# Kernel tuning notes

Hardware: AMD Instinct MI355X
Metric: run time of the kernel (lower is better)

## Reference

```python
import jax, jax.numpy as jnp
import numpy as np

D_MODEL = 1024
NUM_HEADS = 16
HEAD_DIM = D_MODEL // NUM_HEADS


def setup_inputs() -> dict:
    key = jax.random.key(0)
    k_x, k_wqkv, k_bqkv, k_wo, k_bo = jax.random.split(key, 5)
    s = 1.0 / np.sqrt(D_MODEL)
    return {
        "x": jax.random.normal(k_x, (4, 2048, D_MODEL), dtype=jnp.float32),
        "W_qkv": jax.random.uniform(k_wqkv, (D_MODEL, 3 * D_MODEL), jnp.float32, -s, s),
        "b_qkv": jax.random.uniform(k_bqkv, (3 * D_MODEL,), jnp.float32, -s, s),
        "W_out": jax.random.uniform(k_wo, (D_MODEL, D_MODEL), jnp.float32, -s, s),
        "b_out": jax.random.uniform(k_bo, (D_MODEL,), jnp.float32, -s, s),
    }


def reference(x, W_qkv, b_qkv, W_out, b_out):
    B, N, C = x.shape
    # fused QKV projection -> [B, N, 3, H, Dh]
    qkv = (x @ W_qkv + b_qkv).reshape(B, N, 3, NUM_HEADS, HEAD_DIM)
    q = jnp.transpose(qkv[:, :, 0], (0, 2, 1, 3))  # [B, H, N, Dh]
    k = jnp.transpose(qkv[:, :, 1], (0, 2, 1, 3))
    v = jnp.transpose(qkv[:, :, 2], (0, 2, 1, 3))
    scale = 1.0 / jnp.sqrt(jnp.asarray(HEAD_DIM, dtype=x.dtype))
    attn = jnp.einsum('bhqd,bhkd->bhqk', q, k) * scale  # [B, H, N, N]
    attn = jax.nn.softmax(attn, axis=-1)
    # dropout is identity in eval mode
    out = jnp.einsum('bhqk,bhkd->bhqd', attn, v)  # [B, H, N, Dh]
    out = jnp.transpose(out, (0, 2, 1, 3)).reshape(B, N, C)
    return out @ W_out + b_out
```

## Files before the change

### kernel.cpp

```cpp
#include <hip/hip_runtime.h>


typedef __bf16 bf16x8 __attribute__((ext_vector_type(8)));
typedef float f32x4 __attribute__((ext_vector_type(4)));

#define DEV __device__ __forceinline__

DEV unsigned short f2b(float x) {
  unsigned int u = __float_as_uint(x);
  u += 0x7fffu + ((u >> 16) & 1u);
  return (unsigned short)(u >> 16);
}

DEV unsigned int pk_bf16(float a, float b) {
  unsigned int ua = __float_as_uint(a) + 0x8000u;
  unsigned int ub = __float_as_uint(b) + 0x8000u;
  return __builtin_amdgcn_perm(ub, ua, 0x07060302u);
}

#if __has_builtin(__builtin_amdgcn_exp2f)
DEV float exp2_fast(float x) { return __builtin_amdgcn_exp2f(x); }
#else
DEV float exp2_fast(float x) { return exp2f(x); }
#endif

DEV void g2l16(const void* g, void* l) {
  __builtin_amdgcn_global_load_lds(
      (const __attribute__((address_space(1))) unsigned int*)(unsigned long long)g,
      (__attribute__((address_space(3))) unsigned int*)(unsigned int)(unsigned long long)l,
      16, 0, 0);
}

__global__ void cvt_x_kernel(const float* __restrict__ x,
                             unsigned short* __restrict__ xb) {
  int i = blockIdx.x * blockDim.x + threadIdx.x;
  float4 v = ((const float4*)x)[i];
  ushort4 o;
  o.x = f2b(v.x); o.y = f2b(v.y); o.z = f2b(v.z); o.w = f2b(v.w);
  ((ushort4*)xb)[i] = o;
}

__global__ void cvt_wt_kernel(const float* __restrict__ W,
                              unsigned short* __restrict__ Wt,
                              int K, int N) {
  __shared__ float tile[32][33];
  int n0 = blockIdx.x * 32, k0 = blockIdx.y * 32;
  int tx = threadIdx.x, ty = threadIdx.y;
#pragma unroll
  for (int i = 0; i < 32; i += 8)
    tile[ty + i][tx] = W[(size_t)(k0 + ty + i) * N + n0 + tx];
  __syncthreads();
#pragma unroll
  for (int i = 0; i < 32; i += 8)
    Wt[(size_t)(n0 + ty + i) * K + k0 + tx] = f2b(tile[tx][ty + i]);
}

#define QSCALE 0.18033688011112042f

template <int MODE>
__global__ __launch_bounds__(256, 2)
void gemm_bt_kernel(const unsigned short* __restrict__ A,
                    const unsigned short* __restrict__ Bt,
                    const float* __restrict__ bias,
                    unsigned short* __restrict__ qout,
                    unsigned short* __restrict__ kfrout,
                    unsigned short* __restrict__ vfrout,
                    float* __restrict__ fout) {
  constexpr int K = 1024;
  __shared__ unsigned short As[128 * 32];
  __shared__ unsigned short Bs[128 * 32];

  const int tid = threadIdx.x;
  const int lane = tid & 63;
  const int w = tid >> 6;
  const int wm = w & 1, wn = w >> 1;
  const int l15 = lane & 15, quad = lane >> 4;
  const int m0 = blockIdx.y * 128;
  const int n0 = blockIdx.x * 128;

  const unsigned short* Ag = A + (size_t)m0 * K;
  const unsigned short* Bg = Bt + (size_t)n0 * K;

  const int c0 = tid, c1 = tid + 256;
  const size_t ga0 = (size_t)(c0 >> 2) * K + (size_t)(c0 & 3) * 8;
  const size_t ga1 = (size_t)(c1 >> 2) * K + (size_t)(c1 & 3) * 8;
  unsigned short* la0 = &As[c0 * 8];
  unsigned short* la1 = &As[c1 * 8];
  unsigned short* lb0 = &Bs[c0 * 8];
  unsigned short* lb1 = &Bs[c1 * 8];

  f32x4 acc[4][4] = {};

  for (int kt = 0; kt < K; kt += 32) {
    g2l16(Ag + ga0 + kt, la0);
    g2l16(Ag + ga1 + kt, la1);
    g2l16(Bg + ga0 + kt, lb0);
    g2l16(Bg + ga1 + kt, lb1);
    __syncthreads();
    bf16x8 af[4], bfr[4];
#pragma unroll
    for (int i = 0; i < 4; ++i) {
      af[i]  = *(const bf16x8*)&As[(wm * 64 + i * 16 + l15) * 32 + quad * 8];
      bfr[i] = *(const bf16x8*)&Bs[(wn * 64 + i * 16 + l15) * 32 + quad * 8];
    }
#pragma unroll
    for (int mi = 0; mi < 4; ++mi)
#pragma unroll
      for (int ni = 0; ni < 4; ++ni)
        acc[mi][ni] = __builtin_amdgcn_mfma_f32_16x16x32_bf16(
            af[mi], bfr[ni], acc[mi][ni], 0, 0, 0);
    __syncthreads();
  }

  float bv[4];
#pragma unroll
  for (int ni = 0; ni < 4; ++ni)
    bv[ni] = bias[n0 + wn * 64 + ni * 16 + l15];

  if (MODE == 0) {
    const int sel = n0 >> 10;
    const int bbat = m0 >> 11;
    const int ktb = ((m0 & 2047) >> 6) + wm;
    if (sel == 0) {
#pragma unroll
      for (int mi = 0; mi < 4; ++mi) {
        int rb = m0 + wm * 64 + mi * 16 + quad * 4;
#pragma unroll
        for (int ni = 0; ni < 4; ++ni) {
          int c = (n0 & 1023) + wn * 64 + ni * 16 + l15;
#pragma unroll
          for (int r = 0; r < 4; ++r)
            qout[(size_t)(rb + r) * 1024 + c] =
                f2b((acc[mi][ni][r] + bv[ni]) * QSCALE);
        }
      }
    } else if (sel == 1) {
#pragma unroll
      for (int ni = 0; ni < 4; ++ni) {
        int c = (n0 & 1023) + wn * 64 + ni * 16 + l15;
        int h = c >> 6, d = c & 63;
        int kc = d >> 5, dq = (d >> 3) & 3, j = d & 7;
        size_t fb = ((((size_t)(bbat * 16 + h) * 32 + ktb) * 8) + kc) * 512 +
                    (size_t)(dq * 16) * 8 + j;
#pragma unroll
        for (int mi = 0; mi < 4; ++mi) {
          size_t fm = fb + (size_t)mi * 1024;
#pragma unroll
          for (int r = 0; r < 4; ++r)
            kfrout[fm + (quad * 4 + r) * 8] = f2b(acc[mi][ni][r] + bv[ni]);
        }
      }
    } else {
      const int fqb = quad >> 1;
      const int jj0 = (quad & 1) * 4;
#pragma unroll
      for (int ni = 0; ni < 4; ++ni) {
        int c = (n0 & 1023) + wn * 64 + ni * 16 + l15;
        int h = c >> 6, d = c & 63;
        int df = d >> 4, fl15 = d & 15;
#pragma unroll
        for (int mi = 0; mi < 4; ++mi) {
          int kc2 = mi >> 1;
          int fquad = (mi & 1) * 2 + fqb;
          size_t fb = ((((size_t)(bbat * 16 + h) * 32 + ktb) * 8) + df * 2 + kc2) * 512 +
                      (size_t)(fquad * 16 + fl15) * 8 + jj0;
          ushort4 pk;
          pk.x = f2b(acc[mi][ni][0] + bv[ni]);
          pk.y = f2b(acc[mi][ni][1] + bv[ni]);
          pk.z = f2b(acc[mi][ni][2] + bv[ni]);
          pk.w = f2b(acc[mi][ni][3] + bv[ni]);
          *(ushort4*)&vfrout[fb] = pk;
        }
      }
    }
  } else {
#pragma unroll
    for (int mi = 0; mi < 4; ++mi) {
      int rb = m0 + wm * 64 + mi * 16 + quad * 4;
#pragma unroll
      for (int ni = 0; ni < 4; ++ni) {
        int c = n0 + wn * 64 + ni * 16 + l15;
#pragma unroll
        for (int r = 0; r < 4; ++r)
          fout[(size_t)(rb + r) * 1024 + c] = acc[mi][ni][r] + bv[ni];
      }
    }
  }
}

__global__ __launch_bounds__(256, 2)
void attn_kernel(const unsigned short* __restrict__ qg,
                 const unsigned short* __restrict__ kfr,
                 const unsigned short* __restrict__ vfr,
                 unsigned short* __restrict__ oat) {
  __shared__ unsigned short pt[256 * 72];

  const int tid = threadIdx.x;
  const int lane = tid & 63;
  const int w = tid >> 6;
  const int l15 = lane & 15, quad = lane >> 4;

  const int head = blockIdx.x * 8 + (blockIdx.y >> 3);
  const int q0 = (blockIdx.y & 7) * 256;
  const int b = head >> 4, h = head & 15;
  const size_t tokbase = (size_t)b * 2048;

  bf16x8 qf[4][2];
#pragma unroll
  for (int ni = 0; ni < 4; ++ni)
#pragma unroll
    for (int kc = 0; kc < 2; ++kc) {
      int q = q0 + w * 64 + ni * 16 + l15;
      qf[ni][kc] = *(const bf16x8*)(qg + (tokbase + q) * 1024 + h * 64 +
                                    kc * 32 + quad * 8);
    }

  f32x4 oacc[4][4] = {};
  float lsum[4] = {0.f, 0.f, 0.f, 0.f};

  const bf16x8* kp = (const bf16x8*)kfr + (size_t)head * 32 * 512;
  const bf16x8* vp = (const bf16x8*)vfr + (size_t)head * 32 * 512;
  const int qrow = w * 64 + l15;

  bf16x8 kfA[8], vfA[8];
#pragma unroll
  for (int f = 0; f < 8; ++f) {
    kfA[f] = kp[f * 64 + lane];
    vfA[f] = vp[f * 64 + lane];
  }

  for (int kt = 0; kt < 32; ++kt) {
    bf16x8 kfB[8], vfB[8];
    if (kt < 31) {
      const bf16x8* kn = kp + (kt + 1) * 512;
      const bf16x8* vn = vp + (kt + 1) * 512;
#pragma unroll
      for (int f = 0; f < 8; ++f) {
        kfB[f] = kn[f * 64 + lane];
        vfB[f] = vn[f * 64 + lane];
      }
    }

#pragma unroll
    for (int nh = 0; nh < 2; ++nh) {
      f32x4 st[4][2];
#pragma unroll
      for (int mi = 0; mi < 4; ++mi)
#pragma unroll
        for (int nj = 0; nj < 2; ++nj) {
          f32x4 a = {0.f, 0.f, 0.f, 0.f};
          a = __builtin_amdgcn_mfma_f32_16x16x32_bf16(kfA[mi * 2 + 0], qf[nh * 2 + nj][0], a, 0, 0, 0);
          a = __builtin_amdgcn_mfma_f32_16x16x32_bf16(kfA[mi * 2 + 1], qf[nh * 2 + nj][1], a, 0, 0, 0);
          st[mi][nj] = a;
        }
#pragma unroll
      for (int nj = 0; nj < 2; ++nj) {
        int ni = nh * 2 + nj;
        float rs = 0.f;
#pragma unroll
        for (int mi = 0; mi < 4; ++mi) {
          float p0 = exp2_fast(st[mi][nj][0]);
          float p1 = exp2_fast(st[mi][nj][1]);
          float p2 = exp2_fast(st[mi][nj][2]);
          float p3 = exp2_fast(st[mi][nj][3]);
          rs += (p0 + p1) + (p2 + p3);
          uint2 pw;
          pw.x = pk_bf16(p0, p1);
          pw.y = pk_bf16(p2, p3);
          *(uint2*)&pt[(qrow + ni * 16) * 72 + mi * 16 + quad * 4] = pw;
        }
        lsum[ni] += rs;
      }
    }

    bf16x8 pf[4][2];
#pragma unroll
    for (int ni = 0; ni < 4; ++ni)
#pragma unroll
      for (int kc = 0; kc < 2; ++kc)
        pf[ni][kc] = *(const bf16x8*)&pt[(qrow + ni * 16) * 72 + kc * 32 + quad * 8];
#pragma unroll
    for (int df = 0; df < 4; ++df)
#pragma unroll
      for (int kc = 0; kc < 2; ++kc)
#pragma unroll
        for (int ni = 0; ni < 4; ++ni)
          oacc[df][ni] = __builtin_amdgcn_mfma_f32_16x16x32_bf16(
              vfA[df * 2 + kc], pf[ni][kc], oacc[df][ni], 0, 0, 0);

#pragma unroll
    for (int f = 0; f < 8; ++f) { kfA[f] = kfB[f]; vfA[f] = vfB[f]; }
  }

#pragma unroll
  for (int ni = 0; ni < 4; ++ni) {
    float s = lsum[ni];
    s += __shfl_xor(s, 16, 64);
    s += __shfl_xor(s, 32, 64);
    float inv = __builtin_amdgcn_rcpf(s);
    int q = q0 + w * 64 + ni * 16 + l15;
#pragma unroll
    for (int df = 0; df < 4; ++df) {
      uint2 pw;
      pw.x = pk_bf16(oacc[df][ni][0] * inv, oacc[df][ni][1] * inv);
      pw.y = pk_bf16(oacc[df][ni][2] * inv, oacc[df][ni][3] * inv);
      *(uint2*)&oat[(tokbase + q) * 1024 + h * 64 + df * 16 + quad * 4] = pw;
    }
  }
}

extern "C" void kernel_launch(void* const* d_in, const int* in_sizes, int n_in,
                              void* d_out, int out_size, void* d_ws, size_t ws_size,
                              hipStream_t stream) {
  const float* x    = (const float*)d_in[0];
  const float* Wqkv = (const float*)d_in[1];
  const float* bqkv = (const float*)d_in[2];
  const float* Wout = (const float*)d_in[3];
  const float* bout = (const float*)d_in[4];
  float* out = (float*)d_out;

  char* ws = (char*)d_ws;
  unsigned short* xb  = (unsigned short*)(ws + (size_t)0);
  unsigned short* wqt = (unsigned short*)(ws + ((size_t)16 << 20));
  unsigned short* wot = (unsigned short*)(ws + ((size_t)22 << 20));
  unsigned short* qbf = (unsigned short*)(ws + ((size_t)24 << 20));
  unsigned short* kfr = (unsigned short*)(ws + ((size_t)40 << 20));
  unsigned short* vfr = (unsigned short*)(ws + ((size_t)56 << 20));
  unsigned short* oat = (unsigned short*)(ws + ((size_t)72 << 20));

  cvt_x_kernel<<<8192, 256, 0, stream>>>(x, xb);
  cvt_wt_kernel<<<dim3(96, 32), dim3(32, 8), 0, stream>>>(Wqkv, wqt, 1024, 3072);
  cvt_wt_kernel<<<dim3(32, 32), dim3(32, 8), 0, stream>>>(Wout, wot, 1024, 1024);

  gemm_bt_kernel<0><<<dim3(24, 64), 256, 0, stream>>>(
      xb, wqt, bqkv, qbf, kfr, vfr, nullptr);

  attn_kernel<<<dim3(8, 64), 256, 0, stream>>>(qbf, kfr, vfr, oat);

  gemm_bt_kernel<1><<<dim3(8, 64), 256, 0, stream>>>(
      oat, wot, bout, nullptr, nullptr, nullptr, out);
}
```

Measured before the change: 277.6 us.

## Transpose softmax probabilities in registers with permlane swaps instead of LDS

```diff
diff --git a/kernel.cpp b/kernel.cpp
--- a/kernel.cpp
+++ b/kernel.cpp
@@ -3,6 +3,7 @@
 
 typedef __bf16 bf16x8 __attribute__((ext_vector_type(8)));
 typedef float f32x4 __attribute__((ext_vector_type(4)));
+typedef unsigned int u32x4 __attribute__((ext_vector_type(4)));
 
 #define DEV __device__ __forceinline__
 
@@ -23,6 +24,34 @@
 #else
 DEV float exp2_fast(float x) { return exp2f(x); }
 #endif
+
+DEV void xpose_pair(unsigned int a, unsigned int b,
+                    unsigned int& x, unsigned int& y) {
+#if __has_builtin(__builtin_amdgcn_permlane32_swap) && \
+    __has_builtin(__builtin_amdgcn_permlane16_swap)
+  auto t = __builtin_amdgcn_permlane32_swap(a, b, false, false);
+  auto u = __builtin_amdgcn_permlane16_swap(t[0], t[1], false, false);
+  x = u[0];
+  y = u[1];
+#else
+  int la = (int)(threadIdx.x & 63);
+  unsigned int a32 = (unsigned int)__shfl_xor((int)a, 32, 64);
+  unsigned int b32 = (unsigned int)__shfl_xor((int)b, 32, 64);
+  unsigned int t0 = (la < 32) ? a : b32;
+  unsigned int t1 = (la < 32) ? a32 : b;
+  unsigned int t0x = (unsigned int)__shfl_xor((int)t0, 16, 64);
+  unsigned int t1x = (unsigned int)__shfl_xor((int)t1, 16, 64);
+  bool odd = ((la >> 4) & 1) != 0;
+  x = odd ? t1x : t0;
+  y = odd ? t1 : t0x;
+#endif
+}
+
+DEV bf16x8 u4_to_bf(u32x4 v) {
+  union { u32x4 u; bf16x8 b; } c;
+  c.u = v;
+  return c.b;
+}
 
 DEV void g2l16(const void* g, void* l) {
   __builtin_amdgcn_global_load_lds(
@@ -193,8 +222,6 @@
                  const unsigned short* __restrict__ kfr,
                  const unsigned short* __restrict__ vfr,
                  unsigned short* __restrict__ oat) {
-  __shared__ unsigned short pt[256 * 72];
-
   const int tid = threadIdx.x;
   const int lane = tid & 63;
   const int w = tid >> 6;
@@ -220,7 +247,6 @@
 
   const bf16x8* kp = (const bf16x8*)kfr + (size_t)head * 32 * 512;
   const bf16x8* vp = (const bf16x8*)vfr + (size_t)head * 32 * 512;
-  const int qrow = w * 64 + l15;
 
   bf16x8 kfA[8], vfA[8];
 #pragma unroll
@@ -229,6 +255,7 @@
     vfA[f] = vp[f * 64 + lane];
   }
 
+#pragma unroll 2
   for (int kt = 0; kt < 32; ++kt) {
     bf16x8 kfB[8], vfB[8];
     if (kt < 31) {
@@ -247,16 +274,23 @@
 #pragma unroll
       for (int mi = 0; mi < 4; ++mi)
 #pragma unroll
-        for (int nj = 0; nj < 2; ++nj) {
-          f32x4 a = {0.f, 0.f, 0.f, 0.f};
-          a = __builtin_amdgcn_mfma_f32_16x16x32_bf16(kfA[mi * 2 + 0], qf[nh * 2 + nj][0], a, 0, 0, 0);
-          a = __builtin_amdgcn_mfma_f32_16x16x32_bf16(kfA[mi * 2 + 1], qf[nh * 2 + nj][1], a, 0, 0, 0);
-          st[mi][nj] = a;
-        }
+        for (int nj = 0; nj < 2; ++nj)
+          st[mi][nj] = (f32x4){0.f, 0.f, 0.f, 0.f};
+#pragma unroll
+      for (int kc = 0; kc < 2; ++kc)
+#pragma unroll
+        for (int mi = 0; mi < 4; ++mi)
+#pragma unroll
+          for (int nj = 0; nj < 2; ++nj)
+            st[mi][nj] = __builtin_amdgcn_mfma_f32_16x16x32_bf16(
+                kfA[mi * 2 + kc], qf[nh * 2 + nj][kc], st[mi][nj], 0, 0, 0);
+
+      bf16x8 pf2[2][2];
 #pragma unroll
       for (int nj = 0; nj < 2; ++nj) {
         int ni = nh * 2 + nj;
         float rs = 0.f;
+        unsigned int s0[4], s1[4];
 #pragma unroll
         for (int mi = 0; mi < 4; ++mi) {
           float p0 = exp2_fast(st[mi][nj][0]);
@@ -264,29 +298,30 @@
           float p2 = exp2_fast(st[mi][nj][2]);
           float p3 = exp2_fast(st[mi][nj][3]);
           rs += (p0 + p1) + (p2 + p3);
-          uint2 pw;
-          pw.x = pk_bf16(p0, p1);
-          pw.y = pk_bf16(p2, p3);
-          *(uint2*)&pt[(qrow + ni * 16) * 72 + mi * 16 + quad * 4] = pw;
+          s0[mi] = pk_bf16(p0, p1);
+          s1[mi] = pk_bf16(p2, p3);
         }
         lsum[ni] += rs;
-      }
-    }
-
-    bf16x8 pf[4][2];
-#pragma unroll
-    for (int ni = 0; ni < 4; ++ni)
+        unsigned int o00, o01, o02, o03, o10, o11, o12, o13;
+        xpose_pair(s0[0], s0[1], o00, o02);
+        xpose_pair(s1[0], s1[1], o01, o03);
+        xpose_pair(s0[2], s0[3], o10, o12);
+        xpose_pair(s1[2], s1[3], o11, o13);
+        u32x4 t0 = {o00, o01, o02, o03};
+        u32x4 t1 = {o10, o11, o12, o13};
+        pf2[nj][0] = u4_to_bf(t0);
+        pf2[nj][1] = u4_to_bf(t1);
+      }
+
 #pragma unroll
       for (int kc = 0; kc < 2; ++kc)
-        pf[ni][kc] = *(const bf16x8*)&pt[(qrow + ni * 16) * 72 + kc * 32 + quad * 8];
-#pragma unroll
-    for (int df = 0; df < 4; ++df)
-#pragma unroll
-      for (int kc = 0; kc < 2; ++kc)
-#pragma unroll
-        for (int ni = 0; ni < 4; ++ni)
-          oacc[df][ni] = __builtin_amdgcn_mfma_f32_16x16x32_bf16(
-              vfA[df * 2 + kc], pf[ni][kc], oacc[df][ni], 0, 0, 0);
+#pragma unroll
+        for (int df = 0; df < 4; ++df)
+#pragma unroll
+          for (int nj = 0; nj < 2; ++nj)
+            oacc[df][nh * 2 + nj] = __builtin_amdgcn_mfma_f32_16x16x32_bf16(
+                vfA[df * 2 + kc], pf2[nj][kc], oacc[df][nh * 2 + nj], 0, 0, 0);
+    }
 
 #pragma unroll
     for (int f = 0; f < 8; ++f) { kfA[f] = kfB[f]; vfA[f] = vfB[f]; }
```

Result: slower. 332.0 us (+19.6%).
